# Optimization experiments

Hardware: AMD Instinct MI355X
Metric: run time of the kernel (lower is better)

Reference implementation:

```python
import jax, jax.numpy as jnp
import numpy as np

HEADS = 8
DIM_HEAD = 64
SCALE = DIM_HEAD ** (-0.5)


def setup_inputs() -> dict:
    key = jax.random.key(0)
    k1, k2, k3, k4, k5 = jax.random.split(key, 5)
    b, c, h, w = 16, 256, 32, 32
    inner = HEADS * DIM_HEAD  # 512
    return {
        "x": jax.random.normal(k1, (b, c, h, w), dtype=jnp.float32),
        "Wqkv": jax.random.normal(k2, (c, 3 * inner), dtype=jnp.float32) * 0.02,
        "bqkv": jax.random.normal(k3, (3 * inner,), dtype=jnp.float32) * 0.02,
        "Wout": jax.random.normal(k4, (inner, c), dtype=jnp.float32) * 0.02,
        "bout": jax.random.normal(k5, (c,), dtype=jnp.float32) * 0.02,
    }


def reference(x, Wqkv, bqkv, Wout, bout):
    b, c, h, w = x.shape
    n = h * w
    # [b, c, h, w] -> [b, n, c] token-major layout (note: GroupNorm in __init__ is unused in forward)
    xs = jnp.transpose(x.reshape(b, c, n), (0, 2, 1))
    # QKV projection: [b, n, 3*heads*dh] -> [b, n, heads, 3*dh]
    qkv = (xs @ Wqkv + bqkv).reshape(b, n, HEADS, 3 * DIM_HEAD)
    q, k, v = jnp.split(qkv, 3, axis=-1)  # each [b, n, heads, dh]
    # scores [b, i, j, heads], softmax over j (axis=2), as in the original einsum layout
    dots = jnp.einsum("bihd,bjhd->bijh", q, k) * SCALE
    attn = jax.nn.softmax(dots, axis=2)
    res = jnp.einsum("bijh,bjhd->bihd", attn, v).reshape(b, n, HEADS * DIM_HEAD)
    out = res @ Wout + bout + xs  # output proj + residual
    return jnp.transpose(out, (0, 2, 1)).reshape(b, c, h, w)
```

## Files before the change

### kernel.cpp

```cpp
#include <hip/hip_runtime.h>
#include <hip/hip_bf16.h>
#include <stdint.h>

typedef short short8 __attribute__((ext_vector_type(8)));
typedef short bf16x8 __attribute__((ext_vector_type(8)));
typedef float f32x4 __attribute__((ext_vector_type(4)));
typedef float f4 __attribute__((ext_vector_type(4)));
typedef float f32x16 __attribute__((ext_vector_type(16)));
typedef unsigned int u32x2 __attribute__((ext_vector_type(2)));

constexpr int Bn = 16;
constexpr int C  = 256;
constexpr int NT = 1024;
constexpr int NH = 8;
constexpr int INNER = 512;
constexpr int QKVD = 1536;

#define DEVFN __device__ __forceinline__

DEVFN unsigned short f2b_rne(float f) {
    uint32_t x; __builtin_memcpy(&x, &f, 4);
    return (unsigned short)((x + 0x7fffu + ((x >> 16) & 1u)) >> 16);
}
DEVFN float exp2_fast(float x) {
    float r; asm("v_exp_f32 %0, %1" : "=v"(r) : "v"(x)); return r;
}
DEVFN uint32_t cvtpk(float a, float b) {
    uint32_t r; asm("v_cvt_pk_bf16_f32 %0, %1, %2" : "=v"(r) : "v"(a), "v"(b)); return r;
}
DEVFN void permswap(uint32_t& a, uint32_t& b) {
    asm("v_permlane32_swap_b32 %0, %1" : "+v"(a), "+v"(b));
}
DEVFN void gload16(const void* g, void* l) {
    __builtin_amdgcn_global_load_lds((const __attribute__((address_space(1))) void*)g,
                                     (__attribute__((address_space(3))) void*)l, 16, 0, 0);
}

__global__ __launch_bounds__(256) void prep(const float* __restrict__ Wqkv,
                                            const float* __restrict__ Wout,
                                            const float* __restrict__ x,
                                            short* __restrict__ WqkvT,
                                            short* __restrict__ WoutT,
                                            short* __restrict__ xT) {
    __shared__ float T[64][65];
    const int tid = threadIdx.x;
    const int z = blockIdx.z;
    if (z == 0) {
        if (blockIdx.y >= 4) return;
        int jb = blockIdx.x, cb = blockIdx.y;
        int jpb = jb * 64;
        int jorig0 = ((jpb >> 6) & 7) * 192 + (jpb >> 9) * 64;
        #pragma unroll
        for (int it = 0; it < 4; ++it) {
            int cc = (tid >> 4) + it * 16, d4 = (tid & 15) * 4;
            f4 v = *(const f4*)&Wqkv[(size_t)(cb * 64 + cc) * QKVD + jorig0 + d4];
            T[cc][d4] = v[0]; T[cc][d4 + 1] = v[1]; T[cc][d4 + 2] = v[2]; T[cc][d4 + 3] = v[3];
        }
        __syncthreads();
        int d = tid >> 2, cs = tid & 3;
        short8 o0, o1;
        #pragma unroll
        for (int k = 0; k < 8; ++k) o0[k] = (short)f2b_rne(T[cs * 16 + k][d]);
        #pragma unroll
        for (int k = 0; k < 8; ++k) o1[k] = (short)f2b_rne(T[cs * 16 + 8 + k][d]);
        short* orow = WqkvT + (size_t)(jpb + d) * C + cb * 64 + cs * 16;
        *(short8*)orow = o0; *(short8*)(orow + 8) = o1;
    } else if (z == 1) {
        if (blockIdx.x >= 4) return;
        int cb = blockIdx.x, ib = blockIdx.y;
        #pragma unroll
        for (int it = 0; it < 4; ++it) {
            int ii = (tid >> 4) + it * 16, c4 = (tid & 15) * 4;
            f4 v = *(const f4*)&Wout[(size_t)(ib * 64 + ii) * C + cb * 64 + c4];
            T[ii][c4] = v[0]; T[ii][c4 + 1] = v[1]; T[ii][c4 + 2] = v[2]; T[ii][c4 + 3] = v[3];
        }
        __syncthreads();
        int cL = tid >> 2, is = tid & 3;
        short8 o0, o1;
        #pragma unroll
        for (int k = 0; k < 8; ++k) o0[k] = (short)f2b_rne(T[is * 16 + k][cL]);
        #pragma unroll
        for (int k = 0; k < 8; ++k) o1[k] = (short)f2b_rne(T[is * 16 + 8 + k][cL]);
        short* orow = WoutT + (size_t)(cb * 64 + cL) * INNER + ib * 64 + is * 16;
        *(short8*)orow = o0; *(short8*)(orow + 8) = o1;
    } else {
        if (blockIdx.x >= 16 || blockIdx.y >= 4) return;
        int tb = blockIdx.x, cb = blockIdx.y, b = z - 2;
        const float* xb = x + (size_t)b * C * NT;
        #pragma unroll
        for (int it = 0; it < 4; ++it) {
            int cc = (tid >> 4) + it * 16, t4 = (tid & 15) * 4;
            f4 v = *(const f4*)&xb[(size_t)(cb * 64 + cc) * NT + tb * 64 + t4];
            T[cc][t4] = v[0]; T[cc][t4 + 1] = v[1]; T[cc][t4 + 2] = v[2]; T[cc][t4 + 3] = v[3];
        }
        __syncthreads();
        int tL = tid >> 2, cs = tid & 3;
        short8 o0, o1;
        #pragma unroll
        for (int k = 0; k < 8; ++k) o0[k] = (short)f2b_rne(T[cs * 16 + k][tL]);
        #pragma unroll
        for (int k = 0; k < 8; ++k) o1[k] = (short)f2b_rne(T[cs * 16 + 8 + k][tL]);
        short* orow = xT + ((size_t)b * NT + tb * 64 + tL) * C + cb * 64 + cs * 16;
        *(short8*)orow = o0; *(short8*)(orow + 8) = o1;
    }
}

__global__ __launch_bounds__(256) void qkv_gemm(const short* __restrict__ xT,
                                                const short* __restrict__ WqkvT,
                                                const float* __restrict__ bqkv,
                                                short* __restrict__ qkv,
                                                short* __restrict__ Vt) {
    __shared__ __align__(16) short As[128][64];
    __shared__ __align__(16) short Bs[128][64];
    const int tid = threadIdx.x, l = tid & 63, w = tid >> 6;
    const int l15 = l & 15, g = l >> 4;
    const int wr = w >> 1, wc = w & 1;
    const int lr = l >> 3, ls = l & 7;
    const int j0 = blockIdx.x * 128, t0 = blockIdx.y * 128, b = blockIdx.z;
    f32x4 acc[4][4] = {};
    const short* Ab = xT + ((size_t)b * NT + t0) * C;
    const short* Bb = WqkvT + (size_t)j0 * C;

    for (int k0 = 0; k0 < C; k0 += 64) {
        __syncthreads();
        #pragma unroll
        for (int i = 0; i < 4; ++i) {
            int r0 = w * 32 + i * 8;
            int row = r0 + lr;
            int slot = ls ^ (row & 7);
            gload16(Ab + (size_t)row * C + k0 + slot * 8, &As[r0][0]);
            gload16(Bb + (size_t)row * C + k0 + slot * 8, &Bs[r0][0]);
        }
        __syncthreads();
        bf16x8 a[4][2], bb[4][2];
        #pragma unroll
        for (int m = 0; m < 4; ++m) {
            int row = wr * 64 + m * 16 + l15;
            const char* base = (const char*)&As[row][0];
            #pragma unroll
            for (int kk = 0; kk < 2; ++kk)
                a[m][kk] = *(const bf16x8*)(base + (((kk * 4 + g) ^ (row & 7)) << 4));
        }
        #pragma unroll
        for (int n = 0; n < 4; ++n) {
            int row = wc * 64 + n * 16 + l15;
            const char* base = (const char*)&Bs[row][0];
            #pragma unroll
            for (int kk = 0; kk < 2; ++kk)
                bb[n][kk] = *(const bf16x8*)(base + (((kk * 4 + g) ^ (row & 7)) << 4));
        }
        #pragma unroll
        for (int m = 0; m < 4; ++m)
            #pragma unroll
            for (int n = 0; n < 4; ++n) {
                acc[m][n] = __builtin_amdgcn_mfma_f32_16x16x32_bf16(a[m][0], bb[n][0], acc[m][n], 0, 0, 0);
                acc[m][n] = __builtin_amdgcn_mfma_f32_16x16x32_bf16(a[m][1], bb[n][1], acc[m][n], 0, 0, 0);
            }
    }

    if (blockIdx.x < 8) {
        short* qb = qkv + ((size_t)b * NT + t0) * QKVD;
        #pragma unroll
        for (int n = 0; n < 4; ++n) {
            int j = j0 + wc * 64 + n * 16 + l15;
            int jorig = ((j >> 6) & 7) * 192 + (j >> 9) * 64 + (j & 63);
            float bias = bqkv[jorig];
            float scale = (j < 512) ? 0.18033688f : 1.0f;
            #pragma unroll
            for (int m = 0; m < 4; ++m) {
                #pragma unroll
                for (int r = 0; r < 4; ++r) {
                    int t = wr * 64 + m * 16 + g * 4 + r;
                    qb[(size_t)t * QKVD + j] = (short)f2b_rne((acc[m][n][r] + bias) * scale);
                }
            }
        }
    } else {
        short* Vb = Vt + (size_t)b * INNER * NT;
        #pragma unroll
        for (int n = 0; n < 4; ++n) {
            int j = j0 + wc * 64 + n * 16 + l15;
            int jorig = ((j >> 6) & 7) * 192 + (j >> 9) * 64 + (j & 63);
            float bias = bqkv[jorig];
            int vr = j - 1024;
            #pragma unroll
            for (int m = 0; m < 4; ++m) {
                int t = t0 + wr * 64 + m * 16 + g * 4;
                float v0 = acc[m][n][0] + bias, v1 = acc[m][n][1] + bias;
                float v2 = acc[m][n][2] + bias, v3 = acc[m][n][3] + bias;
                u32x2 u; u[0] = cvtpk(v0, v1); u[1] = cvtpk(v2, v3);
                *(u32x2*)(Vb + (size_t)vr * NT + t) = u;
            }
        }
    }
}

__global__ __launch_bounds__(256, 2) void attn(const short* __restrict__ qkv,
                                               const short* __restrict__ Vt,
                                               short* __restrict__ res) {
    __shared__ __align__(16) short Kl[3][64][64];
    __shared__ __align__(16) short Vl[3][64][64];
    const int tid = threadIdx.x, l = tid & 63, w = tid >> 6;
    const int q31 = l & 31, hi = l >> 5;
    const int lr = l >> 3, ls = l & 7;
    const int bid = blockIdx.x;
    const int work = (bid & 7) * 64 + (bid >> 3);
    const int pair = work >> 2, qq = work & 3;
    const int b = pair >> 3, h = pair & 7;

    const short* Kg = qkv + (size_t)b * NT * QKVD + 512 + h * 64;
    const short* Vg = Vt + ((size_t)b * INNER + h * 64) * NT;

    bf16x8 qf[2][4];
    #pragma unroll
    for (int qb2 = 0; qb2 < 2; ++qb2) {
        int q = qq * 256 + w * 64 + qb2 * 32 + q31;
        const short* Qr = qkv + ((size_t)b * NT + q) * QKVD + h * 64 + hi * 8;
        #pragma unroll
        for (int s = 0; s < 4; ++s) qf[qb2][s] = *(const bf16x8*)(Qr + 16 * s);
    }

    f32x16 sumAcc[2] = {};
    f32x16 o[2][2] = {};

    #define STAGE(tile, buf)                                                              \
        {                                                                                 \
            int k0s = (tile) * 64;                                                        \
            _Pragma("unroll")                                                             \
            for (int i = 0; i < 2; ++i) {                                                 \
                int r0 = w * 16 + i * 8;                                                  \
                int row = r0 + lr;                                                        \
                gload16(Kg + (size_t)(k0s + row) * QKVD + (ls ^ lr) * 8, &Kl[buf][r0][0]);\
                gload16(Vg + (size_t)row * NT + k0s + (ls ^ lr) * 8, &Vl[buf][r0][0]);    \
            }                                                                             \
        }

    STAGE(0, 0)
    STAGE(1, 1)

    for (int t = 0; t < 16; ++t) {
        if (t < 15) asm volatile("s_waitcnt vmcnt(4)" ::: "memory");
        else        asm volatile("s_waitcnt vmcnt(0)" ::: "memory");
        __builtin_amdgcn_s_barrier();
        const int buf = t % 3;
        const char* kb = (const char*)&Kl[buf][0][0];
        const char* vb = (const char*)&Vl[buf][0][0];

        if (t < 14) STAGE(t + 2, (t + 2) % 3)

        bf16x8 kf[2][4], vf[2][4];
        #pragma unroll
        for (int kb2 = 0; kb2 < 2; ++kb2)
            #pragma unroll
            for (int s = 0; s < 4; ++s)
                kf[kb2][s] = *(const bf16x8*)(kb + (kb2 * 32 + q31) * 128 + (((s * 2 + hi) ^ (q31 & 7)) << 4));
        #pragma unroll
        for (int db = 0; db < 2; ++db)
            #pragma unroll
            for (int kc = 0; kc < 4; ++kc)
                vf[db][kc] = *(const bf16x8*)(vb + (db * 32 + q31) * 128 + (((kc * 2 + hi) ^ (q31 & 7)) << 4));

        #pragma unroll
        for (int qb2 = 0; qb2 < 2; ++qb2) {
            f32x16 st0 = {}, st1 = {};
            __builtin_amdgcn_s_setprio(1);
            #pragma unroll
            for (int s = 0; s < 4; ++s) {
                st0 = __builtin_amdgcn_mfma_f32_32x32x16_bf16(kf[0][s], qf[qb2][s], st0, 0, 0, 0);
                st1 = __builtin_amdgcn_mfma_f32_32x32x16_bf16(kf[1][s], qf[qb2][s], st1, 0, 0, 0);
            }
            __builtin_amdgcn_s_setprio(0);
            #pragma unroll
            for (int r = 0; r < 16; ++r) {
                st0[r] = exp2_fast(st0[r]);
                st1[r] = exp2_fast(st1[r]);
            }
            #pragma unroll
            for (int r = 0; r < 16; ++r) sumAcc[qb2][r] += st0[r] + st1[r];

            bf16x8 pa[4];
            #pragma unroll
            for (int kc = 0; kc < 4; ++kc) {
                uint32_t w0, w1, w2, w3;
                if (kc < 2) {
                    const int i0 = (kc & 1) * 8;
                    w0 = cvtpk(st0[i0 + 0], st0[i0 + 1]); w2 = cvtpk(st0[i0 + 4], st0[i0 + 5]);
                    w1 = cvtpk(st0[i0 + 2], st0[i0 + 3]); w3 = cvtpk(st0[i0 + 6], st0[i0 + 7]);
                } else {
                    const int i0 = (kc & 1) * 8;
                    w0 = cvtpk(st1[i0 + 0], st1[i0 + 1]); w2 = cvtpk(st1[i0 + 4], st1[i0 + 5]);
                    w1 = cvtpk(st1[i0 + 2], st1[i0 + 3]); w3 = cvtpk(st1[i0 + 6], st1[i0 + 7]);
                }
                permswap(w0, w2); permswap(w1, w3);
                uint32_t pw[4] = {w0, w1, w2, w3};
                __builtin_memcpy(&pa[kc], pw, 16);
            }
            __builtin_amdgcn_s_setprio(1);
            #pragma unroll
            for (int kc = 0; kc < 4; ++kc) {
                o[qb2][0] = __builtin_amdgcn_mfma_f32_32x32x16_bf16(vf[0][kc], pa[kc], o[qb2][0], 0, 0, 0);
                o[qb2][1] = __builtin_amdgcn_mfma_f32_32x32x16_bf16(vf[1][kc], pa[kc], o[qb2][1], 0, 0, 0);
            }
            __builtin_amdgcn_s_setprio(0);
        }
    }
    #undef STAGE

    #pragma unroll
    for (int qb2 = 0; qb2 < 2; ++qb2) {
        float sm[16];
        #pragma unroll
        for (int r = 0; r < 16; ++r) sm[r] = sumAcc[qb2][r];
        #pragma unroll
        for (int stp = 8; stp > 0; stp >>= 1)
            #pragma unroll
            for (int r = 0; r < stp; ++r) sm[r] += sm[r + stp];
        float lR = sm[0] + __shfl_xor(sm[0], 32, 64);
        const float inv = 1.0f / lR;
        int q = qq * 256 + w * 64 + qb2 * 32 + q31;
        short* rb = res + ((size_t)b * NT + q) * INNER + h * 64 + hi * 4;
        #pragma unroll
        for (int g2 = 0; g2 < 4; ++g2) {
            u32x2 u;
            u[0] = cvtpk(o[qb2][0][4 * g2 + 0] * inv, o[qb2][0][4 * g2 + 1] * inv);
            u[1] = cvtpk(o[qb2][0][4 * g2 + 2] * inv, o[qb2][0][4 * g2 + 3] * inv);
            *(u32x2*)(rb + 8 * g2) = u;
            u32x2 u2;
            u2[0] = cvtpk(o[qb2][1][4 * g2 + 0] * inv, o[qb2][1][4 * g2 + 1] * inv);
            u2[1] = cvtpk(o[qb2][1][4 * g2 + 2] * inv, o[qb2][1][4 * g2 + 3] * inv);
            *(u32x2*)(rb + 32 + 8 * g2) = u2;
        }
    }
}

__global__ __launch_bounds__(256) void out_proj(const short* __restrict__ WoutT,
                                                const short* __restrict__ res,
                                                const float* __restrict__ bout,
                                                const float* __restrict__ x,
                                                float* __restrict__ out) {
    __shared__ __align__(16) short As[128][64];
    __shared__ __align__(16) short Bs[128][64];
    const int tid = threadIdx.x, l = tid & 63, w = tid >> 6;
    const int l15 = l & 15, g = l >> 4;
    const int wr = w >> 1, wc = w & 1;
    const int lr = l >> 3, ls = l & 7;
    const int t0 = blockIdx.x * 128, c0 = blockIdx.y * 128, b = blockIdx.z;
    f32x4 acc[4][4] = {};
    const short* Ab = WoutT + (size_t)c0 * INNER;
    const short* Bb = res + ((size_t)b * NT + t0) * INNER;

    for (int k0 = 0; k0 < INNER; k0 += 64) {
        __syncthreads();
        #pragma unroll
        for (int i = 0; i < 4; ++i) {
            int r0 = w * 32 + i * 8;
            int row = r0 + lr;
            int slot = ls ^ (row & 7);
            gload16(Ab + (size_t)row * INNER + k0 + slot * 8, &As[r0][0]);
            gload16(Bb + (size_t)row * INNER + k0 + slot * 8, &Bs[r0][0]);
        }
        __syncthreads();
        bf16x8 a[4][2], bb[4][2];
        #pragma unroll
        for (int m = 0; m < 4; ++m) {
            int row = wr * 64 + m * 16 + l15;
            const char* base = (const char*)&As[row][0];
            #pragma unroll
            for (int kk = 0; kk < 2; ++kk)
                a[m][kk] = *(const bf16x8*)(base + (((kk * 4 + g) ^ (row & 7)) << 4));
        }
        #pragma unroll
        for (int n = 0; n < 4; ++n) {
            int row = wc * 64 + n * 16 + l15;
            const char* base = (const char*)&Bs[row][0];
            #pragma unroll
            for (int kk = 0; kk < 2; ++kk)
                bb[n][kk] = *(const bf16x8*)(base + (((kk * 4 + g) ^ (row & 7)) << 4));
        }
        #pragma unroll
        for (int m = 0; m < 4; ++m)
            #pragma unroll
            for (int n = 0; n < 4; ++n) {
                acc[m][n] = __builtin_amdgcn_mfma_f32_16x16x32_bf16(a[m][0], bb[n][0], acc[m][n], 0, 0, 0);
                acc[m][n] = __builtin_amdgcn_mfma_f32_16x16x32_bf16(a[m][1], bb[n][1], acc[m][n], 0, 0, 0);
            }
    }

    const float* xb = x + (size_t)b * C * NT;
    float* ob = out + (size_t)b * C * NT;
    #pragma unroll
    for (int m = 0; m < 4; ++m) {
        #pragma unroll
        for (int r = 0; r < 4; ++r) {
            int c = c0 + wr * 64 + m * 16 + g * 4 + r;
            float bias = bout[c];
            #pragma unroll
            for (int n = 0; n < 4; ++n) {
                int t = t0 + wc * 64 + n * 16 + l15;
                size_t idx = (size_t)c * NT + t;
                ob[idx] = acc[m][n][r] + bias + xb[idx];
            }
        }
    }
}

extern "C" void kernel_launch(void* const* d_in, const int* in_sizes, int n_in,
                              void* d_out, int out_size, void* d_ws, size_t ws_size,
                              hipStream_t stream) {
    const float* x    = (const float*)d_in[0];
    const float* Wqkv = (const float*)d_in[1];
    const float* bqkv = (const float*)d_in[2];
    const float* Wout = (const float*)d_in[3];
    const float* bout = (const float*)d_in[4];
    float* out = (float*)d_out;

    char* ws = (char*)d_ws;
    short* qkvb  = (short*)(ws);
    short* VtB   = (short*)(ws + 50331648);
    short* xTres = (short*)(ws + 67108864);
    short* WqT   = (short*)(ws + 83886080);
    short* WoT   = (short*)(ws + 84672512);

    prep<<<dim3(24, 8, 18), 256, 0, stream>>>(Wqkv, Wout, x, WqT, WoT, xTres);
    qkv_gemm<<<dim3(12, 8, 16), 256, 0, stream>>>(xTres, WqT, bqkv, qkvb, VtB);
    attn<<<dim3(512, 1, 1), 256, 0, stream>>>(qkvb, VtB, xTres);
    out_proj<<<dim3(8, 2, 16), 256, 0, stream>>>(WoT, xTres, bout, x, out);
}
```

Before: 98.87 us.

## Split attention work across 8 waves with 32 queries each

The attention kernel now runs 512 threads per block, and each wave handles 32 queries instead of 64. This halves per-wave register state (Q fragments, accumulators, row sums) and allows higher occupancy under launch bounds of 4 blocks. K/V staging is spread over 8 waves with one load each, and the waitcnt is adjusted to match. Each K/V tile read from LDS is now reused over fewer queries per wave, and the setprio hints are removed, which may reduce MFMA density.

```diff
diff --git a/kernel.cpp b/kernel.cpp
--- a/kernel.cpp
+++ b/kernel.cpp
@@ -6,6 +6,7 @@
 typedef short bf16x8 __attribute__((ext_vector_type(8)));
 typedef float f32x4 __attribute__((ext_vector_type(4)));
 typedef float f4 __attribute__((ext_vector_type(4)));
+typedef float f32x8 __attribute__((ext_vector_type(8)));
 typedef float f32x16 __attribute__((ext_vector_type(16)));
 typedef unsigned int u32x2 __attribute__((ext_vector_type(2)));
 
@@ -195,7 +196,7 @@
     }
 }
 
-__global__ __launch_bounds__(256, 2) void attn(const short* __restrict__ qkv,
+__global__ __launch_bounds__(512, 4) void attn(const short* __restrict__ qkv,
                                                const short* __restrict__ Vt,
                                                short* __restrict__ res) {
     __shared__ __align__(16) short Kl[3][64][64];
@@ -211,35 +212,30 @@
     const short* Kg = qkv + (size_t)b * NT * QKVD + 512 + h * 64;
     const short* Vg = Vt + ((size_t)b * INNER + h * 64) * NT;
 
-    bf16x8 qf[2][4];
-    #pragma unroll
-    for (int qb2 = 0; qb2 < 2; ++qb2) {
-        int q = qq * 256 + w * 64 + qb2 * 32 + q31;
+    bf16x8 qf[4];
+    {
+        int q = qq * 256 + w * 32 + q31;
         const short* Qr = qkv + ((size_t)b * NT + q) * QKVD + h * 64 + hi * 8;
         #pragma unroll
-        for (int s = 0; s < 4; ++s) qf[qb2][s] = *(const bf16x8*)(Qr + 16 * s);
-    }
-
-    f32x16 sumAcc[2] = {};
-    f32x16 o[2][2] = {};
+        for (int s = 0; s < 4; ++s) qf[s] = *(const bf16x8*)(Qr + 16 * s);
+    }
+
+    f32x8 sumAcc = {};
+    f32x16 o0 = {}, o1 = {};
 
     #define STAGE(tile, buf)                                                              \
         {                                                                                 \
             int k0s = (tile) * 64;                                                        \
-            _Pragma("unroll")                                                             \
-            for (int i = 0; i < 2; ++i) {                                                 \
-                int r0 = w * 16 + i * 8;                                                  \
-                int row = r0 + lr;                                                        \
-                gload16(Kg + (size_t)(k0s + row) * QKVD + (ls ^ lr) * 8, &Kl[buf][r0][0]);\
-                gload16(Vg + (size_t)row * NT + k0s + (ls ^ lr) * 8, &Vl[buf][r0][0]);    \
-            }                                                                             \
+            int row = w * 8 + lr;                                                         \
+            gload16(Kg + (size_t)(k0s + row) * QKVD + (ls ^ lr) * 8, &Kl[buf][w * 8][0]); \
+            gload16(Vg + (size_t)row * NT + k0s + (ls ^ lr) * 8, &Vl[buf][w * 8][0]);     \
         }
 
     STAGE(0, 0)
     STAGE(1, 1)
 
     for (int t = 0; t < 16; ++t) {
-        if (t < 15) asm volatile("s_waitcnt vmcnt(4)" ::: "memory");
+        if (t < 15) asm volatile("s_waitcnt vmcnt(2)" ::: "memory");
         else        asm volatile("s_waitcnt vmcnt(0)" ::: "memory");
         __builtin_amdgcn_s_barrier();
         const int buf = t % 3;
@@ -248,88 +244,76 @@
 
         if (t < 14) STAGE(t + 2, (t + 2) % 3)
 
-        bf16x8 kf[2][4], vf[2][4];
-        #pragma unroll
-        for (int kb2 = 0; kb2 < 2; ++kb2)
-            #pragma unroll
-            for (int s = 0; s < 4; ++s)
-                kf[kb2][s] = *(const bf16x8*)(kb + (kb2 * 32 + q31) * 128 + (((s * 2 + hi) ^ (q31 & 7)) << 4));
-        #pragma unroll
-        for (int db = 0; db < 2; ++db)
-            #pragma unroll
-            for (int kc = 0; kc < 4; ++kc)
-                vf[db][kc] = *(const bf16x8*)(vb + (db * 32 + q31) * 128 + (((kc * 2 + hi) ^ (q31 & 7)) << 4));
-
-        #pragma unroll
-        for (int qb2 = 0; qb2 < 2; ++qb2) {
-            f32x16 st0 = {}, st1 = {};
-            __builtin_amdgcn_s_setprio(1);
-            #pragma unroll
-            for (int s = 0; s < 4; ++s) {
-                st0 = __builtin_amdgcn_mfma_f32_32x32x16_bf16(kf[0][s], qf[qb2][s], st0, 0, 0, 0);
-                st1 = __builtin_amdgcn_mfma_f32_32x32x16_bf16(kf[1][s], qf[qb2][s], st1, 0, 0, 0);
-            }
-            __builtin_amdgcn_s_setprio(0);
-            #pragma unroll
-            for (int r = 0; r < 16; ++r) {
-                st0[r] = exp2_fast(st0[r]);
-                st1[r] = exp2_fast(st1[r]);
-            }
-            #pragma unroll
-            for (int r = 0; r < 16; ++r) sumAcc[qb2][r] += st0[r] + st1[r];
-
-            bf16x8 pa[4];
-            #pragma unroll
-            for (int kc = 0; kc < 4; ++kc) {
-                uint32_t w0, w1, w2, w3;
-                if (kc < 2) {
-                    const int i0 = (kc & 1) * 8;
-                    w0 = cvtpk(st0[i0 + 0], st0[i0 + 1]); w2 = cvtpk(st0[i0 + 4], st0[i0 + 5]);
-                    w1 = cvtpk(st0[i0 + 2], st0[i0 + 3]); w3 = cvtpk(st0[i0 + 6], st0[i0 + 7]);
-                } else {
-                    const int i0 = (kc & 1) * 8;
-                    w0 = cvtpk(st1[i0 + 0], st1[i0 + 1]); w2 = cvtpk(st1[i0 + 4], st1[i0 + 5]);
-                    w1 = cvtpk(st1[i0 + 2], st1[i0 + 3]); w3 = cvtpk(st1[i0 + 6], st1[i0 + 7]);
-                }
-                permswap(w0, w2); permswap(w1, w3);
-                uint32_t pw[4] = {w0, w1, w2, w3};
-                __builtin_memcpy(&pa[kc], pw, 16);
-            }
-            __builtin_amdgcn_s_setprio(1);
-            #pragma unroll
-            for (int kc = 0; kc < 4; ++kc) {
-                o[qb2][0] = __builtin_amdgcn_mfma_f32_32x32x16_bf16(vf[0][kc], pa[kc], o[qb2][0], 0, 0, 0);
-                o[qb2][1] = __builtin_amdgcn_mfma_f32_32x32x16_bf16(vf[1][kc], pa[kc], o[qb2][1], 0, 0, 0);
-            }
-            __builtin_amdgcn_s_setprio(0);
+        bf16x8 kf0[4], kf1[4];
+        #pragma unroll
+        for (int s = 0; s < 4; ++s) {
+            kf0[s] = *(const bf16x8*)(kb + q31 * 128 + (((s * 2 + hi) ^ (q31 & 7)) << 4));
+            kf1[s] = *(const bf16x8*)(kb + (32 + q31) * 128 + (((s * 2 + hi) ^ (q31 & 7)) << 4));
+        }
+        f32x16 s0 = {}, s1 = {};
+        #pragma unroll
+        for (int s = 0; s < 4; ++s) {
+            s0 = __builtin_amdgcn_mfma_f32_32x32x16_bf16(kf0[s], qf[s], s0, 0, 0, 0);
+            s1 = __builtin_amdgcn_mfma_f32_32x32x16_bf16(kf1[s], qf[s], s1, 0, 0, 0);
+        }
+        bf16x8 vf0[4], vf1[4];
+        #pragma unroll
+        for (int kc = 0; kc < 4; ++kc) {
+            vf0[kc] = *(const bf16x8*)(vb + q31 * 128 + (((kc * 2 + hi) ^ (q31 & 7)) << 4));
+            vf1[kc] = *(const bf16x8*)(vb + (32 + q31) * 128 + (((kc * 2 + hi) ^ (q31 & 7)) << 4));
+        }
+
+        #pragma unroll
+        for (int r = 0; r < 16; ++r) { s0[r] = exp2_fast(s0[r]); s1[r] = exp2_fast(s1[r]); }
+        #pragma unroll
+        for (int r = 0; r < 8; ++r) sumAcc[r] += (s0[r] + s0[r + 8]) + (s1[r] + s1[r + 8]);
+
+        bf16x8 pa[4];
+        #pragma unroll
+        for (int kc = 0; kc < 4; ++kc) {
+            uint32_t w0, w1, w2, w3;
+            if (kc < 2) {
+                const int i0 = (kc & 1) * 8;
+                w0 = cvtpk(s0[i0 + 0], s0[i0 + 1]); w2 = cvtpk(s0[i0 + 4], s0[i0 + 5]);
+                w1 = cvtpk(s0[i0 + 2], s0[i0 + 3]); w3 = cvtpk(s0[i0 + 6], s0[i0 + 7]);
+            } else {
+                const int i0 = (kc & 1) * 8;
+                w0 = cvtpk(s1[i0 + 0], s1[i0 + 1]); w2 = cvtpk(s1[i0 + 4], s1[i0 + 5]);
+                w1 = cvtpk(s1[i0 + 2], s1[i0 + 3]); w3 = cvtpk(s1[i0 + 6], s1[i0 + 7]);
+            }
+            permswap(w0, w2); permswap(w1, w3);
+            uint32_t pw[4] = {w0, w1, w2, w3};
+            __builtin_memcpy(&pa[kc], pw, 16);
+        }
+        #pragma unroll
+        for (int kc = 0; kc < 4; ++kc) {
+            o0 = __builtin_amdgcn_mfma_f32_32x32x16_bf16(vf0[kc], pa[kc], o0, 0, 0, 0);
+            o1 = __builtin_amdgcn_mfma_f32_32x32x16_bf16(vf1[kc], pa[kc], o1, 0, 0, 0);
         }
     }
     #undef STAGE
 
+    float sm[8];
     #pragma unroll
-    for (int qb2 = 0; qb2 < 2; ++qb2) {
-        float sm[16];
-        #pragma unroll
-        for (int r = 0; r < 16; ++r) sm[r] = sumAcc[qb2][r];
-        #pragma unroll
-        for (int stp = 8; stp > 0; stp >>= 1)
-            #pragma unroll
-            for (int r = 0; r < stp; ++r) sm[r] += sm[r + stp];
-        float lR = sm[0] + __shfl_xor(sm[0], 32, 64);
-        const float inv = 1.0f / lR;
-        int q = qq * 256 + w * 64 + qb2 * 32 + q31;
-        short* rb = res + ((size_t)b * NT + q) * INNER + h * 64 + hi * 4;
-        #pragma unroll
-        for (int g2 = 0; g2 < 4; ++g2) {
-            u32x2 u;
-            u[0] = cvtpk(o[qb2][0][4 * g2 + 0] * inv, o[qb2][0][4 * g2 + 1] * inv);
-            u[1] = cvtpk(o[qb2][0][4 * g2 + 2] * inv, o[qb2][0][4 * g2 + 3] * inv);
-            *(u32x2*)(rb + 8 * g2) = u;
-            u32x2 u2;
-            u2[0] = cvtpk(o[qb2][1][4 * g2 + 0] * inv, o[qb2][1][4 * g2 + 1] * inv);
-            u2[1] = cvtpk(o[qb2][1][4 * g2 + 2] * inv, o[qb2][1][4 * g2 + 3] * inv);
-            *(u32x2*)(rb + 32 + 8 * g2) = u2;
-        }
+    for (int r = 0; r < 8; ++r) sm[r] = sumAcc[r];
+    #pragma unroll
+    for (int stp = 4; stp > 0; stp >>= 1)
+        #pragma unroll
+        for (int r = 0; r < stp; ++r) sm[r] += sm[r + stp];
+    float lR = sm[0] + __shfl_xor(sm[0], 32, 64);
+    const float inv = 1.0f / lR;
+    int q = qq * 256 + w * 32 + q31;
+    short* rb = res + ((size_t)b * NT + q) * INNER + h * 64 + hi * 4;
+    #pragma unroll
+    for (int g2 = 0; g2 < 4; ++g2) {
+        u32x2 u;
+        u[0] = cvtpk(o0[4 * g2 + 0] * inv, o0[4 * g2 + 1] * inv);
+        u[1] = cvtpk(o0[4 * g2 + 2] * inv, o0[4 * g2 + 3] * inv);
+        *(u32x2*)(rb + 8 * g2) = u;
+        u32x2 u2;
+        u2[0] = cvtpk(o1[4 * g2 + 0] * inv, o1[4 * g2 + 1] * inv);
+        u2[1] = cvtpk(o1[4 * g2 + 2] * inv, o1[4 * g2 + 3] * inv);
+        *(u32x2*)(rb + 32 + 8 * g2) = u2;
     }
 }
 
@@ -423,6 +407,6 @@
 
     prep<<<dim3(24, 8, 18), 256, 0, stream>>>(Wqkv, Wout, x, WqT, WoT, xTres);
     qkv_gemm<<<dim3(12, 8, 16), 256, 0, stream>>>(xTres, WqT, bqkv, qkvb, VtB);
-    attn<<<dim3(512, 1, 1), 256, 0, stream>>>(qkvb, VtB, xTres);
+    attn<<<dim3(512, 1, 1), 512, 0, stream>>>(qkvb, VtB, xTres);
     out_proj<<<dim3(8, 2, 16), 256, 0, stream>>>(WoT, xTres, bout, x, out);
 }
```

Measured after the change: 96.37 us. 2.5% less time.
